# Optimization experiments

Measured on AMD Instinct MI355X. Metric: run time of the kernel, lower is better.

The kernel has to match this reference:

```python
import jax, jax.numpy as jnp
import numpy as np

B, I, C, H, QP, VP = 2, 1024, 16, 12, 4, 8
W_C = (2.0 / (9.0 * QP)) ** 0.5
W_L = (1.0 / 3.0) ** 0.5


def setup_inputs() -> dict:
    key = jax.random.key(0)
    ks = jax.random.split(key, 14)
    rn = lambda k, shape, s=1.0: (jax.random.normal(k, shape, dtype=jnp.float32) * s)
    return {
        "s": rn(ks[0], (B, I, C)),
        "z": rn(ks[1], (B, I, I, C)),
        "R": rn(ks[2], (B, I, 3, 3)),
        "t": rn(ks[3], (B, I, 3)),
        "Wq": rn(ks[4], (C, C * H), C ** -0.5),
        "Wk": rn(ks[5], (C, C * H), C ** -0.5),
        "Wv": rn(ks[6], (C, C * H), C ** -0.5),
        "Wb": rn(ks[7], (C, H), C ** -0.5),
        "Wqp": rn(ks[8], (C, 3 * QP * H), C ** -0.5),
        "Wkp": rn(ks[9], (C, 3 * QP * H), C ** -0.5),
        "Wvp": rn(ks[10], (C, 3 * VP * H), C ** -0.5),
        "gamma": rn(ks[11], (H,), 0.5),
        "Wout": rn(ks[12], (H * (2 * C + 4 * VP), C), (H * (2 * C + 4 * VP)) ** -0.5),
        "bout": rn(ks[13], (C,), 0.02),
    }


def _apply_rigid(R, t, p):
    # p: (B, i, n, 3); rigid transform per residue: R @ p + t
    return jnp.einsum("bixy,bipy->bipx", R, p) + t[:, :, None, :]


def reference(s, z, R, t, Wq, Wk, Wv, Wb, Wqp, Wkp, Wvp, gamma, Wout, bout):
    b_, i_, c = s.shape
    h, qp, vp = gamma.shape[0], Wqp.shape[1] // (3 * gamma.shape[0]), Wvp.shape[1] // (3 * gamma.shape[0])

    q = (s @ Wq).reshape(b_, i_, h, c)
    k = (s @ Wk).reshape(b_, i_, h, c)
    v = (s @ Wv).reshape(b_, i_, h, c)

    q_pts = _apply_rigid(R, t, (s @ Wqp).reshape(b_, i_, h * qp, 3)).reshape(b_, i_, h, qp, 3)
    k_pts = _apply_rigid(R, t, (s @ Wkp).reshape(b_, i_, h * qp, 3)).reshape(b_, i_, h, qp, 3)
    v_pts = _apply_rigid(R, t, (s @ Wvp).reshape(b_, i_, h * vp, 3)).reshape(b_, i_, h, vp, 3)

    bias = jnp.einsum("bijc,ch->bhij", z, Wb)
    a = jnp.einsum("bihc,bjhc->bhij", q, k) * (c ** -0.5) + bias

    # squared point distances summed over points, expanded to avoid (B,i,j,h,P,3) tensor
    q2 = jnp.sum(q_pts ** 2, axis=(-1, -2))          # (B,i,h)
    k2 = jnp.sum(k_pts ** 2, axis=(-1, -2))          # (B,j,h)
    qk = jnp.einsum("bihpx,bjhpx->bhij", q_pts, k_pts)
    d2 = q2.transpose(0, 2, 1)[..., None] + k2.transpose(0, 2, 1)[:, :, None, :] - 2.0 * qk  # (B,h,i,j)

    head_w = jax.nn.softplus(gamma)                  # (h,)
    a = a + d2 * (head_w[None, :, None, None] * W_C * -0.5)
    a = a * W_L
    a = jax.nn.softmax(a, axis=-2)  # NOTE: original code softmaxes over dim=-2 (the i axis)

    # NOTE: original einsum indexes v by i (not j); replicated faithfully
    o = jnp.einsum("bhij,bihc->bihc", a, v).reshape(b_, i_, h * c)

    o_pts = jnp.einsum("bhij,bjhpx->bihpx", a, v_pts)  # (B,i,h,vp,3)
    o_pts_norm = jnp.sqrt(jnp.maximum(jnp.sum(o_pts ** 2, axis=-1), 1e-12)).reshape(b_, i_, h * vp)
    o_pts_flat = o_pts.reshape(b_, i_, h * vp * 3)

    o_pair = jnp.einsum("bhij,bijc->bihc", a, z).reshape(b_, i_, h * c)

    cat = jnp.concatenate([o, o_pair, o_pts_flat, o_pts_norm], axis=-1)
    return cat @ Wout + bout
```

## Files before the change

kernel.cpp:

```cpp
#include <hip/hip_runtime.h>
#include <hip/hip_bf16.h>
#include <math.h>

#define B_ 2
#define I_ 1024
#define C_ 16
#define H_ 12
#define ICH 16

__device__ __constant__ float kW_C = 0.23570226039551584f;
#define W_Lc 0.5773502691896258f
#define LOG2E 1.4426950408889634f

typedef _Float16 hf;
typedef hf hf2 __attribute__((ext_vector_type(2)));
typedef hf hf4v __attribute__((ext_vector_type(4)));
typedef hf hf8v __attribute__((ext_vector_type(8)));
typedef float f32x4 __attribute__((ext_vector_type(4)));
typedef unsigned int u32;

template <typename T, typename F>
__device__ inline T bc(F f) { return __builtin_bit_cast(T, f); }

__device__ inline float fdot2f(u32 a, u32 b, float c) {
#if __has_builtin(__builtin_amdgcn_fdot2)
  return __builtin_amdgcn_fdot2(bc<hf2>(a), bc<hf2>(b), c, false);
#else
  hf2 x = bc<hf2>(a), y = bc<hf2>(b);
  return c + (float)x[0] * (float)y[0] + (float)x[1] * (float)y[1];
#endif
}

__device__ inline u32 pkrtz(float lo, float hi) {
#if __has_builtin(__builtin_amdgcn_cvt_pkrtz)
  return bc<u32>(__builtin_amdgcn_cvt_pkrtz(lo, hi));
#else
  hf2 t; t[0] = (hf)lo; t[1] = (hf)hi; return bc<u32>(t);
#endif
}

__device__ inline u32 permlo(u32 hiw, u32 low) {
#if __has_builtin(__builtin_amdgcn_perm)
  return __builtin_amdgcn_perm(hiw, low, 0x05040100u);
#else
  return (low & 0xffffu) | (hiw << 16);
#endif
}
__device__ inline u32 permhi(u32 hiw, u32 low) {
#if __has_builtin(__builtin_amdgcn_perm)
  return __builtin_amdgcn_perm(hiw, low, 0x07060302u);
#else
  return (low >> 16) | (hiw & 0xffff0000u);
#endif
}

#define QF16_OFF 0
#define QF16_SZ (B_*I_*196)
#define KF16_OFF (QF16_OFF + QF16_SZ)
#define KF16_SZ QF16_SZ
#define VPF_OFF (KF16_OFF + KF16_SZ)
#define VPF_SZ (B_*I_*144)
#define VV_OFF (VPF_OFF + VPF_SZ)
#define VV_SZ (B_*I_*192)
#define SM_OFF (VV_OFF + VV_SZ)
#define SM_SZ (B_*12*1024*2)
#define PM_OFF (SM_OFF + SM_SZ)
#define PM_SZ (B_*64*ICH*192*2)
#define LT_OFF (PM_OFF + PM_SZ)
#define LT_SZ (B_*H_*512*1024)
#define ACC2_OFF (LT_OFF + LT_SZ)

__global__ __launch_bounds__(192) void kA(const float* __restrict__ s, const float* __restrict__ R,
                 const float* __restrict__ t, const float* __restrict__ Wq,
                 const float* __restrict__ Wk, const float* __restrict__ Wv,
                 const float* __restrict__ Wqp, const float* __restrict__ Wkp,
                 const float* __restrict__ Wvp, const float* __restrict__ gam,
                 float* __restrict__ ws) {
  int blk = blockIdx.x;
  int b = blk >> 10, i = blk & 1023;
  int tid = threadIdx.x;
  __shared__ float sl[16], rl[9], tl[3], part[96];
  if (tid < 16) sl[tid] = s[(b*I_ + i)*C_ + tid];
  else if (tid < 25) rl[tid-16] = R[(size_t)(b*I_+i)*9 + (tid-16)];
  else if (tid < 28) tl[tid-25] = t[(size_t)(b*I_+i)*3 + (tid-25)];
  __syncthreads();
  hf* QF  = (hf*)(ws + QF16_OFF) + (size_t)(b*I_+i)*392;
  hf* KF  = (hf*)(ws + KF16_OFF) + (size_t)(b*I_+i)*392;
  ushort* VPP = (ushort*)(ws + VPF_OFF);
  float* vv = ws + VV_OFF + (size_t)(b*I_+i)*192;
  {
    int hc = tid; int h = hc >> 4, c = hc & 15;
    float aq = 0.f, ak = 0.f, av = 0.f;
    #pragma unroll
    for (int ci = 0; ci < 16; ci++) {
      float sv = sl[ci];
      aq += sv * Wq[ci*192 + hc];
      ak += sv * Wk[ci*192 + hc];
      av += sv * Wv[ci*192 + hc];
    }
    const float s_qk = 0.25f * W_Lc * LOG2E;
    QF[h*32 + c] = (hf)(aq * s_qk);
    KF[h*32 + c] = (hf)ak;
    vv[hc] = av;
  }
  {
    float raw[3], px[3];
    if (tid < 96) {
      bool isq = tid < 48;
      int n = isq ? tid : tid - 48;
      const float* W = isq ? Wqp : Wkp;
      #pragma unroll
      for (int x = 0; x < 3; x++) {
        float a2 = 0.f;
        #pragma unroll
        for (int ci = 0; ci < 16; ci++) a2 += sl[ci] * W[ci*144 + n*3 + x];
        raw[x] = a2;
      }
      #pragma unroll
      for (int x = 0; x < 3; x++)
        px[x] = rl[x*3]*raw[0] + rl[x*3+1]*raw[1] + rl[x*3+2]*raw[2] + tl[x];
      int h = n >> 2, p = n & 3;
      part[tid] = px[0]*px[0] + px[1]*px[1] + px[2]*px[2];
      if (isq) {
        float g = gam[h];
        float sp = log1pf(expf(g));
        float coef2 = -0.5f * kW_C * sp * W_Lc * LOG2E;
        #pragma unroll
        for (int x = 0; x < 3; x++) QF[h*32 + 16 + p*3 + x] = (hf)(px[x] * (-2.0f * coef2));
      } else {
        #pragma unroll
        for (int x = 0; x < 3; x++) KF[h*32 + 16 + p*3 + x] = (hf)px[x];
      }
    } else {
      int n = tid - 96;
      #pragma unroll
      for (int x = 0; x < 3; x++) {
        float a2 = 0.f;
        #pragma unroll
        for (int ci = 0; ci < 16; ci++) a2 += sl[ci] * Wvp[ci*288 + n*3 + x];
        raw[x] = a2;
      }
      #pragma unroll
      for (int x = 0; x < 3; x++)
        px[x] = rl[x*3]*raw[0] + rl[x*3+1]*raw[1] + rl[x*3+2]*raw[2] + tl[x];
      int h = n >> 3, p = n & 7;
      size_t base = ((size_t)(b*512 + (i >> 1))*12 + h)*48 + (i & 1);
      #pragma unroll
      for (int x = 0; x < 3; x++) VPP[base + (p*3 + x)*2] = bc<ushort>((hf)px[x]);
    }
  }
  __syncthreads();
  if (tid < 24) {
    int h = tid % 12; bool isq = tid < 12;
    float g = gam[h];
    float sp = log1pf(expf(g));
    float coef2 = -0.5f * kW_C * sp * W_Lc * LOG2E;
    float s2 = 0.f;
    int base = isq ? h*4 : 48 + h*4;
    #pragma unroll
    for (int p = 0; p < 4; p++) s2 += part[base + p];
    if (isq) {
      QF[h*32 + 28] = (hf)(coef2 * s2);
      QF[h*32 + 29] = (hf)1.0f;
      QF[h*32 + 30] = (hf)0.0f;
      QF[h*32 + 31] = (hf)0.0f;
    } else {
      KF[h*32 + 28] = (hf)1.0f;
      KF[h*32 + 29] = (hf)(coef2 * s2);
      KF[h*32 + 30] = (hf)0.0f;
      KF[h*32 + 31] = (hf)0.0f;
    }
  }
}

__global__ __launch_bounds__(256,6) void kB(const float* __restrict__ z,
                 const float* __restrict__ Wb, float* __restrict__ ws) {
  int blk = blockIdx.x;
  int ic = blk & (ICH-1); int jt = (blk >> 4) & 63; int b = blk >> 10;
  int tid = threadIdx.x;
  int w = tid >> 6, lane = tid & 63;
  int ln15 = lane & 15, l16 = lane >> 4;
  int j0 = jt*16;
  __shared__ u32 lqk[12*16*18];
  __shared__ u32 lbias32[16*112];
  const ushort* QFu = (const ushort*)(ws + QF16_OFF);
  const ushort* KFu = (const ushort*)(ws + KF16_OFF);
  hf8v kf[3];
  #pragma unroll
  for (int q = 0; q < 3; q++) {
    int h = w*3 + q;
    kf[q] = *(const hf8v*)&KFu[(size_t)(b*I_ + j0 + ln15)*392 + h*32 + l16*8];
  }
  hf4v wbf;
  #pragma unroll
  for (int e = 0; e < 4; e++) {
    int c = l16*4 + e;
    float v = (ln15 < 12) ? Wb[c*12 + ln15] * (W_Lc*LOG2E) : 0.f;
    wbf[e] = (hf)v;
  }
  u32* LTu_w = (u32*)(ws + LT_OFF);
  float m = -1e30f, S = 0.f;
  float4 zb0, zb1, zb2, zb3;
  {
    const float* zbase = z + ((size_t)(b*I_ + ic*64 + w*4)*I_ + j0 + ln15)*16 + l16*4;
    zb0 = *(const float4*)(zbase);
    zb1 = *(const float4*)(zbase + (size_t)I_*16);
    zb2 = *(const float4*)(zbase + (size_t)I_*32);
    zb3 = *(const float4*)(zbase + (size_t)I_*48);
  }
  for (int t = 0; t < 4; ++t) {
    int i0 = ic*64 + t*16;
    #pragma unroll
    for (int q = 0; q < 3; q++) {
      int h = w*3 + q;
      hf8v a = *(const hf8v*)&QFu[(size_t)(b*I_ + i0 + ln15)*392 + h*32 + l16*8];
      f32x4 c = {0.f, 0.f, 0.f, 0.f};
      c = __builtin_amdgcn_mfma_f32_16x16x32_f16(a, kf[q], c, 0, 0, 0);
      u32* dst = &lqk[(h*16 + ln15)*18 + l16*4];
      *(uint2*)dst     = make_uint2(bc<u32>(c[0]), bc<u32>(c[1]));
      *(uint2*)(dst+2) = make_uint2(bc<u32>(c[2]), bc<u32>(c[3]));
    }
    #pragma unroll
    for (int r = 0; r < 4; r++) {
      float4 zv = (r == 0) ? zb0 : (r == 1) ? zb1 : (r == 2) ? zb2 : zb3;
      int ii = w*4 + r;
      uint2 ap = make_uint2(pkrtz(zv.x, zv.y), pkrtz(zv.z, zv.w));
      hf4v a = bc<hf4v>(ap);
      f32x4 cb = {0.f, 0.f, 0.f, 0.f};
      cb = __builtin_amdgcn_mfma_f32_16x16x16f16(a, wbf, cb, 0, 0, 0);
      if (ln15 < 12) {
        u32 b01 = pkrtz(cb[0], cb[1]);
        u32 b23 = pkrtz(cb[2], cb[3]);
        *(uint2*)&lbias32[ii*112 + ln15*9 + l16*2] = make_uint2(b01, b23);
      }
    }
    if (t < 3) {
      const float* zbase = z + ((size_t)(b*I_ + ic*64 + (t+1)*16 + w*4)*I_ + j0 + ln15)*16 + l16*4;
      zb0 = *(const float4*)(zbase);
      zb1 = *(const float4*)(zbase + (size_t)I_*16);
      zb2 = *(const float4*)(zbase + (size_t)I_*32);
      zb3 = *(const float4*)(zbase + (size_t)I_*48);
    }
    __syncthreads();
    if (tid < 192) {
      int h = tid >> 4, jl = tid & 15;
      const u32* qk = &lqk[(h*16 + jl)*18];
      float l[16];
      #pragma unroll
      for (int i = 0; i < 16; i++) {
        u32 bb = lbias32[i*112 + h*9 + (jl >> 1)];
        ushort bu = (jl & 1) ? (ushort)(bb >> 16) : (ushort)(bb & 0xffffu);
        l[i] = bc<float>(qk[i]) + (float)bc<hf>(bu);
      }
      u32 lw[8];
      #pragma unroll
      for (int p = 0; p < 8; p++) lw[p] = pkrtz(l[2*p], l[2*p+1]);
      float lr[16];
      #pragma unroll
      for (int p = 0; p < 8; p++) { hf2 lh = bc<hf2>(lw[p]); lr[2*p] = (float)lh[0]; lr[2*p+1] = (float)lh[1]; }
      float m8[8];
      #pragma unroll
      for (int p = 0; p < 8; p++) m8[p] = fmaxf(lr[2*p], lr[2*p+1]);
      float mt = fmaxf(fmaxf(fmaxf(m8[0],m8[1]), fmaxf(m8[2],m8[3])),
                       fmaxf(fmaxf(m8[4],m8[5]), fmaxf(m8[6],m8[7])));
      float e[16];
      #pragma unroll
      for (int p = 0; p < 16; p++) e[p] = __builtin_amdgcn_exp2f(lr[p] - mt);
      float st = ((e[0]+e[1])+(e[2]+e[3])) + ((e[4]+e[5])+(e[6]+e[7]))
               + ((e[8]+e[9])+(e[10]+e[11])) + ((e[12]+e[13])+(e[14]+e[15]));
      float mn = fmaxf(m, mt);
      S = S * __builtin_amdgcn_exp2f(m - mn) + st * __builtin_amdgcn_exp2f(mt - mn);
      m = mn;
      u32 ex[8];
      #pragma unroll
      for (int p = 0; p < 8; p++) {
        u32 pw = (u32)__shfl_xor((int)lw[p], 1);
        ex[p] = (jl & 1) ? permhi(lw[p], pw) : permlo(pw, lw[p]);
      }
      u32 sw[8];
      #pragma unroll
      for (int p = 0; p < 8; p++) sw[p] = (u32)__shfl_xor((int)ex[p], 1);
      int par = jl & 1;
      u32 o0 = par ? sw[4] : ex[0];
      u32 o1 = par ? ex[4] : sw[0];
      u32 o2 = par ? sw[5] : ex[1];
      u32 o3 = par ? ex[5] : sw[1];
      u32 o4 = par ? sw[6] : ex[2];
      u32 o5 = par ? ex[6] : sw[2];
      u32 o6 = par ? sw[7] : ex[3];
      u32 o7 = par ? ex[7] : sw[3];
      u32* dst = LTu_w + ((size_t)(b*12+h)*512 + jt*8 + (jl>>1))*1024 + i0 + par*8;
      *(uint4*)dst     = make_uint4(o0, o1, o2, o3);
      *(uint4*)(dst+4) = make_uint4(o4, o5, o6, o7);
    }
    __syncthreads();
  }
  if (tid < 192) {
    float2* pm = (float2*)(ws + PM_OFF);
    pm[((size_t)(b*64+jt)*ICH + ic)*192 + tid] = make_float2(m, S);
  }
}

__global__ __launch_bounds__(192) void kB2(float* __restrict__ ws) {
  int blk = blockIdx.x; int jt = blk & 63, b = blk >> 6;
  int tid = threadIdx.x; int h = tid >> 4, jl = tid & 15;
  const float2* pm = (const float2*)(ws + PM_OFF) + (size_t)(b*64+jt)*ICH*192 + tid;
  float m = -1e30f, S = 0.f;
  #pragma unroll
  for (int ic = 0; ic < ICH; ic++) {
    float2 p = pm[ic*192];
    float mn = fmaxf(m, p.x);
    S = S * __builtin_amdgcn_exp2f(m - mn) + p.y * __builtin_amdgcn_exp2f(p.x - mn);
    m = mn;
  }
  int j = jt*16 + jl;
  float* sm = ws + SM_OFF + ((size_t)((b*12+h)*1024) + j)*2;
  sm[0] = m;
  sm[1] = 1.0f / S;
}

__global__ __launch_bounds__(192,6) void kC(const float* __restrict__ z,
                 float* __restrict__ ws, int jsh) {
  int blk = blockIdx.x;
  int jch = 1 << jsh;
  int jc = blk & (jch-1); int it = (blk >> jsh) & 63; int b = blk >> (jsh+6);
  int tid = threadIdx.x; int h = tid >> 4, il = tid & 15;
  int i = it*16 + il;
  __shared__ u32 llds[96*18];
  __shared__ u32 zplds[16*132];
  float opts[24], opair[16], rsum = 0.f;
  #pragma unroll
  for (int n = 0; n < 24; n++) opts[n] = 0.f;
  #pragma unroll
  for (int c = 0; c < 16; c++) opair[c] = 0.f;
  const u32* LTu = (const u32*)(ws + LT_OFF);
  const float* SM = ws + SM_OFF + (size_t)((b*12+h)*1024)*2;
  const ushort* VPP = (const ushort*)(ws + VPF_OFF);
  int chunk = I_ >> jsh;
  int nt = chunk >> 4;
  int hh = tid >> 4, rr = tid & 15, sjp = rr >> 1, sq = rr & 1;
  for (int t = 0; t < nt; ++t) {
    int j0 = jc*chunk + t*16;
    int jpg0 = j0 >> 1;
    __syncthreads();
    {
      const u32* src = LTu + ((size_t)(b*12+hh)*512 + jpg0 + sjp)*1024 + it*16 + sq*8;
      uint4 a = *(const uint4*)src;
      uint4 c4 = *(const uint4*)(src + 4);
      u32* drow = llds + (hh*8 + sjp)*18 + sq*8;
      *(uint2*)(drow + 0) = make_uint2(a.x, a.y);
      *(uint2*)(drow + 2) = make_uint2(a.z, a.w);
      *(uint2*)(drow + 4) = make_uint2(c4.x, c4.y);
      *(uint2*)(drow + 6) = make_uint2(c4.z, c4.w);
    }
    for (int idx = tid; idx < 512; idx += 192) {
      int r = idx >> 5, jp = (idx >> 2) & 7, c4 = idx & 3;
      const float* zb = z + ((size_t)(b*I_ + it*16 + r)*I_ + j0 + 2*jp)*16 + c4*4;
      float4 a = *(const float4*)zb;
      float4 d = *(const float4*)(zb + 16);
      uint4 o = make_uint4(pkrtz(a.x, d.x), pkrtz(a.y, d.y), pkrtz(a.z, d.z), pkrtz(a.w, d.w));
      *(uint4*)&zplds[r*132 + jp*16 + c4*4] = o;
    }
    __syncthreads();
    #pragma unroll 1
    for (int jp = 0; jp < 8; ++jp) {
      u32 lp = llds[(h*8 + jp)*18 + il];
      float4 st = *(const float4*)(SM + (size_t)(j0 + 2*jp)*2);
      const uint4* vp4 = (const uint4*)(VPP + ((size_t)(b*512 + jpg0 + jp)*12 + h)*48);
      uint4 va = vp4[0], vb = vp4[1], vc = vp4[2];
      uint4 vd = vp4[3], ve = vp4[4], vf = vp4[5];
      hf2 lh = bc<hf2>(lp);
      float w0 = __builtin_amdgcn_exp2f((float)lh[0] - st.x) * st.y;
      float w1 = __builtin_amdgcn_exp2f((float)lh[1] - st.z) * st.w;
      rsum += w0 + w1;
      u32 w2 = pkrtz(w0, w1);
      const u32* zr = &zplds[il*132 + jp*16];
      uint4 p0 = *(const uint4*)(zr + 0), p1 = *(const uint4*)(zr + 4);
      uint4 p2 = *(const uint4*)(zr + 8), p3 = *(const uint4*)(zr + 12);
      opair[0]  = fdot2f(w2, p0.x, opair[0]);
      opair[1]  = fdot2f(w2, p0.y, opair[1]);
      opair[2]  = fdot2f(w2, p0.z, opair[2]);
      opair[3]  = fdot2f(w2, p0.w, opair[3]);
      opair[4]  = fdot2f(w2, p1.x, opair[4]);
      opair[5]  = fdot2f(w2, p1.y, opair[5]);
      opair[6]  = fdot2f(w2, p1.z, opair[6]);
      opair[7]  = fdot2f(w2, p1.w, opair[7]);
      opair[8]  = fdot2f(w2, p2.x, opair[8]);
      opair[9]  = fdot2f(w2, p2.y, opair[9]);
      opair[10] = fdot2f(w2, p2.z, opair[10]);
      opair[11] = fdot2f(w2, p2.w, opair[11]);
      opair[12] = fdot2f(w2, p3.x, opair[12]);
      opair[13] = fdot2f(w2, p3.y, opair[13]);
      opair[14] = fdot2f(w2, p3.z, opair[14]);
      opair[15] = fdot2f(w2, p3.w, opair[15]);
      opts[0]  = fdot2f(w2, va.x, opts[0]);
      opts[1]  = fdot2f(w2, va.y, opts[1]);
      opts[2]  = fdot2f(w2, va.z, opts[2]);
      opts[3]  = fdot2f(w2, va.w, opts[3]);
      opts[4]  = fdot2f(w2, vb.x, opts[4]);
      opts[5]  = fdot2f(w2, vb.y, opts[5]);
      opts[6]  = fdot2f(w2, vb.z, opts[6]);
      opts[7]  = fdot2f(w2, vb.w, opts[7]);
      opts[8]  = fdot2f(w2, vc.x, opts[8]);
      opts[9]  = fdot2f(w2, vc.y, opts[9]);
      opts[10] = fdot2f(w2, vc.z, opts[10]);
      opts[11] = fdot2f(w2, vc.w, opts[11]);
      opts[12] = fdot2f(w2, vd.x, opts[12]);
      opts[13] = fdot2f(w2, vd.y, opts[13]);
      opts[14] = fdot2f(w2, vd.z, opts[14]);
      opts[15] = fdot2f(w2, vd.w, opts[15]);
      opts[16] = fdot2f(w2, ve.x, opts[16]);
      opts[17] = fdot2f(w2, ve.y, opts[17]);
      opts[18] = fdot2f(w2, ve.z, opts[18]);
      opts[19] = fdot2f(w2, ve.w, opts[19]);
      opts[20] = fdot2f(w2, vf.x, opts[20]);
      opts[21] = fdot2f(w2, vf.y, opts[21]);
      opts[22] = fdot2f(w2, vf.z, opts[22]);
      opts[23] = fdot2f(w2, vf.w, opts[23]);
    }
  }
  ushort* ab = (ushort*)(ws + ACC2_OFF) + ((size_t)(b*I_+i)*jch + jc)*512;
  #pragma unroll
  for (int n = 0; n < 24; n++) ab[h*24 + n] = bc<ushort>((hf)opts[n]);
  #pragma unroll
  for (int c = 0; c < 16; c++) ab[288 + h*16 + c] = bc<ushort>((hf)opair[c]);
  ab[480 + h] = bc<ushort>((hf)rsum);
}

__global__ __launch_bounds__(256) void kD(const float* __restrict__ Wout, const float* __restrict__ bout,
                 const float* __restrict__ ws, float* __restrict__ out, int jsh) {
  int jch = 1 << jsh;
  int blk = blockIdx.x;
  int b = blk >> 8; int i0 = (blk & 255) << 2;
  int tid = threadIdx.x;
  __shared__ float accs[4*512];
  __shared__ float cat[4*776];
  __shared__ float red[256];
  const ushort* ACC2us = (const ushort*)(ws + ACC2_OFF);
  for (int idx = tid; idx < 4*512; idx += 256) {
    int r = idx >> 9, f = idx & 511;
    const ushort* src = ACC2us + (size_t)(b*I_+i0+r)*jch*512 + f;
    float ssum = 0.f;
    for (int jc = 0; jc < jch; jc++) ssum += (float)bc<hf>(src[jc*512]);
    accs[idx] = ssum;
  }
  __syncthreads();
  const float* vv = ws + VV_OFF;
  for (int idx = tid; idx < 4*768; idx += 256) {
    int r = idx / 768, f = idx - r*768;
    int i = i0 + r;
    const float* ab = accs + r*512;
    float val;
    if (f < 192) {
      int h = f >> 4, c = f & 15;
      val = vv[(size_t)(b*I_+i)*192 + h*16 + c] * ab[480 + h];
    } else if (f < 384) {
      val = ab[288 + (f - 192)];
    } else if (f < 672) {
      val = ab[f - 384];
    } else {
      int g = f - 672; int base = (g >> 3)*24 + (g & 7)*3;
      float x0 = ab[base], x1 = ab[base+1], x2 = ab[base+2];
      val = sqrtf(fmaxf(x0*x0 + x1*x1 + x2*x2, 1e-12f));
    }
    cat[r*776 + f] = val;
  }
  __syncthreads();
  {
    int r = tid >> 6, c = (tid >> 2) & 15, sseg = tid & 3;
    const float* cr = cat + r*776;
    float a = 0.f;
    for (int f = sseg*192; f < sseg*192 + 192; f++) a += cr[f] * Wout[f*16 + c];
    red[tid] = a;
  }
  __syncthreads();
  if ((tid & 3) == 0) {
    int r = tid >> 6, c = (tid >> 2) & 15;
    float sum = bout[c] + red[tid] + red[tid+1] + red[tid+2] + red[tid+3];
    out[((size_t)(b*I_) + i0 + r)*16 + c] = sum;
  }
}

extern "C" void kernel_launch(void* const* d_in, const int* in_sizes, int n_in,
                              void* d_out, int out_size, void* d_ws, size_t ws_size,
                              hipStream_t stream) {
  const float* s    = (const float*)d_in[0];
  const float* z    = (const float*)d_in[1];
  const float* R    = (const float*)d_in[2];
  const float* t    = (const float*)d_in[3];
  const float* Wq   = (const float*)d_in[4];
  const float* Wk   = (const float*)d_in[5];
  const float* Wv   = (const float*)d_in[6];
  const float* Wb   = (const float*)d_in[7];
  const float* Wqp  = (const float*)d_in[8];
  const float* Wkp  = (const float*)d_in[9];
  const float* Wvp  = (const float*)d_in[10];
  const float* gam  = (const float*)d_in[11];
  const float* Wout = (const float*)d_in[12];
  const float* bout = (const float*)d_in[13];
  float* out = (float*)d_out;
  float* ws = (float*)d_ws;

  int jsh = 4;
  while (jsh > 0) {
    size_t need = ((size_t)ACC2_OFF + (size_t)B_*I_*(1u<<jsh)*256) * 4u;
    if (need <= ws_size) break;
    jsh--;
  }

  hipLaunchKernelGGL(kA, dim3(B_*I_), dim3(192), 0, stream,
                     s, R, t, Wq, Wk, Wv, Wqp, Wkp, Wvp, gam, ws);
  hipLaunchKernelGGL(kB, dim3(B_*64*ICH), dim3(256), 0, stream, z, Wb, ws);
  hipLaunchKernelGGL(kB2, dim3(B_*64), dim3(192), 0, stream, ws);
  hipLaunchKernelGGL(kC, dim3(B_*64*(1<<jsh)), dim3(192), 0, stream, z, ws, jsh);
  hipLaunchKernelGGL(kD, dim3(B_*256), dim3(256), 0, stream, Wout, bout, ws, out, jsh);
}
```

Measured before the change: 180.0 us.

## Double-buffer LDS tiles in kC with register prefetch of next z/logit tile

kC now keeps two LDS buffers for the logit and z tiles. The next tile's global loads are issued into registers before the current tile's compute loop and written to the other buffer afterward. This overlaps global memory latency with the dot-product work and removes one barrier per iteration. It lowers the launch-bounds occupancy hint from 6 to 3 to make room for the extra prefetch registers, and it unrolls the inner loop by 2, at the cost of fewer resident waves and double the LDS use.

```diff
diff --git a/kernel.cpp b/kernel.cpp
--- a/kernel.cpp
+++ b/kernel.cpp
@@ -319,15 +319,15 @@
   sm[1] = 1.0f / S;
 }
 
-__global__ __launch_bounds__(192,6) void kC(const float* __restrict__ z,
+__global__ __launch_bounds__(192,3) void kC(const float* __restrict__ z,
                  float* __restrict__ ws, int jsh) {
   int blk = blockIdx.x;
   int jch = 1 << jsh;
   int jc = blk & (jch-1); int it = (blk >> jsh) & 63; int b = blk >> (jsh+6);
   int tid = threadIdx.x; int h = tid >> 4, il = tid & 15;
   int i = it*16 + il;
-  __shared__ u32 llds[96*18];
-  __shared__ u32 zplds[16*132];
+  __shared__ u32 llds[2][96*18];
+  __shared__ u32 zplds[2][16*132];
   float opts[24], opair[16], rsum = 0.f;
   #pragma unroll
   for (int n = 0; n < 24; n++) opts[n] = 0.f;
@@ -339,32 +339,60 @@
   int chunk = I_ >> jsh;
   int nt = chunk >> 4;
   int hh = tid >> 4, rr = tid & 15, sjp = rr >> 1, sq = rr & 1;
+  int x0r = tid >> 5,        x0jp = (tid >> 2) & 7,        x0c = tid & 3;
+  int x1r = (tid+192) >> 5,  x1jp = ((tid+192) >> 2) & 7,  x1c = (tid+192) & 3;
+  int x2r = (tid+384) >> 5,  x2jp = ((tid+384) >> 2) & 7,  x2c = (tid+384) & 3;
+  uint4 lta, ltb;
+  float4 za0, zd0, za1, zd1, za2, zd2;
+  {
+    int j0 = jc*chunk;
+    int jpg0 = j0 >> 1;
+    const u32* src = LTu + ((size_t)(b*12+hh)*512 + jpg0 + sjp)*1024 + it*16 + sq*8;
+    lta = *(const uint4*)src;
+    ltb = *(const uint4*)(src + 4);
+    const float* zb0p = z + ((size_t)(b*I_ + it*16 + x0r)*I_ + j0 + 2*x0jp)*16 + x0c*4;
+    za0 = *(const float4*)zb0p; zd0 = *(const float4*)(zb0p + 16);
+    const float* zb1p = z + ((size_t)(b*I_ + it*16 + x1r)*I_ + j0 + 2*x1jp)*16 + x1c*4;
+    za1 = *(const float4*)zb1p; zd1 = *(const float4*)(zb1p + 16);
+    if (tid < 128) {
+      const float* zb2p = z + ((size_t)(b*I_ + it*16 + x2r)*I_ + j0 + 2*x2jp)*16 + x2c*4;
+      za2 = *(const float4*)zb2p; zd2 = *(const float4*)(zb2p + 16);
+    }
+    u32* drow = llds[0] + (hh*8 + sjp)*18 + sq*8;
+    *(uint2*)(drow + 0) = make_uint2(lta.x, lta.y);
+    *(uint2*)(drow + 2) = make_uint2(lta.z, lta.w);
+    *(uint2*)(drow + 4) = make_uint2(ltb.x, ltb.y);
+    *(uint2*)(drow + 6) = make_uint2(ltb.z, ltb.w);
+    *(uint4*)&zplds[0][x0r*132 + x0jp*16 + x0c*4] =
+      make_uint4(pkrtz(za0.x, zd0.x), pkrtz(za0.y, zd0.y), pkrtz(za0.z, zd0.z), pkrtz(za0.w, zd0.w));
+    *(uint4*)&zplds[0][x1r*132 + x1jp*16 + x1c*4] =
+      make_uint4(pkrtz(za1.x, zd1.x), pkrtz(za1.y, zd1.y), pkrtz(za1.z, zd1.z), pkrtz(za1.w, zd1.w));
+    if (tid < 128)
+      *(uint4*)&zplds[0][x2r*132 + x2jp*16 + x2c*4] =
+        make_uint4(pkrtz(za2.x, zd2.x), pkrtz(za2.y, zd2.y), pkrtz(za2.z, zd2.z), pkrtz(za2.w, zd2.w));
+    __syncthreads();
+  }
   for (int t = 0; t < nt; ++t) {
+    int cur = t & 1;
     int j0 = jc*chunk + t*16;
     int jpg0 = j0 >> 1;
-    __syncthreads();
-    {
-      const u32* src = LTu + ((size_t)(b*12+hh)*512 + jpg0 + sjp)*1024 + it*16 + sq*8;
-      uint4 a = *(const uint4*)src;
-      uint4 c4 = *(const uint4*)(src + 4);
-      u32* drow = llds + (hh*8 + sjp)*18 + sq*8;
-      *(uint2*)(drow + 0) = make_uint2(a.x, a.y);
-      *(uint2*)(drow + 2) = make_uint2(a.z, a.w);
-      *(uint2*)(drow + 4) = make_uint2(c4.x, c4.y);
-      *(uint2*)(drow + 6) = make_uint2(c4.z, c4.w);
-    }
-    for (int idx = tid; idx < 512; idx += 192) {
-      int r = idx >> 5, jp = (idx >> 2) & 7, c4 = idx & 3;
-      const float* zb = z + ((size_t)(b*I_ + it*16 + r)*I_ + j0 + 2*jp)*16 + c4*4;
-      float4 a = *(const float4*)zb;
-      float4 d = *(const float4*)(zb + 16);
-      uint4 o = make_uint4(pkrtz(a.x, d.x), pkrtz(a.y, d.y), pkrtz(a.z, d.z), pkrtz(a.w, d.w));
-      *(uint4*)&zplds[r*132 + jp*16 + c4*4] = o;
-    }
-    __syncthreads();
-    #pragma unroll 1
+    if (t + 1 < nt) {
+      int j1 = j0 + 16;
+      const u32* src = LTu + ((size_t)(b*12+hh)*512 + (j1>>1) + sjp)*1024 + it*16 + sq*8;
+      lta = *(const uint4*)src;
+      ltb = *(const uint4*)(src + 4);
+      const float* zb0p = z + ((size_t)(b*I_ + it*16 + x0r)*I_ + j1 + 2*x0jp)*16 + x0c*4;
+      za0 = *(const float4*)zb0p; zd0 = *(const float4*)(zb0p + 16);
+      const float* zb1p = z + ((size_t)(b*I_ + it*16 + x1r)*I_ + j1 + 2*x1jp)*16 + x1c*4;
+      za1 = *(const float4*)zb1p; zd1 = *(const float4*)(zb1p + 16);
+      if (tid < 128) {
+        const float* zb2p = z + ((size_t)(b*I_ + it*16 + x2r)*I_ + j1 + 2*x2jp)*16 + x2c*4;
+        za2 = *(const float4*)zb2p; zd2 = *(const float4*)(zb2p + 16);
+      }
+    }
+    #pragma unroll 2
     for (int jp = 0; jp < 8; ++jp) {
-      u32 lp = llds[(h*8 + jp)*18 + il];
+      u32 lp = llds[cur][(h*8 + jp)*18 + il];
       float4 st = *(const float4*)(SM + (size_t)(j0 + 2*jp)*2);
       const uint4* vp4 = (const uint4*)(VPP + ((size_t)(b*512 + jpg0 + jp)*12 + h)*48);
       uint4 va = vp4[0], vb = vp4[1], vc = vp4[2];
@@ -374,7 +402,7 @@
       float w1 = __builtin_amdgcn_exp2f((float)lh[1] - st.z) * st.w;
       rsum += w0 + w1;
       u32 w2 = pkrtz(w0, w1);
-      const u32* zr = &zplds[il*132 + jp*16];
+      const u32* zr = &zplds[cur][il*132 + jp*16];
       uint4 p0 = *(const uint4*)(zr + 0), p1 = *(const uint4*)(zr + 4);
       uint4 p2 = *(const uint4*)(zr + 8), p3 = *(const uint4*)(zr + 12);
       opair[0]  = fdot2f(w2, p0.x, opair[0]);
@@ -418,6 +446,22 @@
       opts[22] = fdot2f(w2, vf.z, opts[22]);
       opts[23] = fdot2f(w2, vf.w, opts[23]);
     }
+    if (t + 1 < nt) {
+      int nb = cur ^ 1;
+      u32* drow = llds[nb] + (hh*8 + sjp)*18 + sq*8;
+      *(uint2*)(drow + 0) = make_uint2(lta.x, lta.y);
+      *(uint2*)(drow + 2) = make_uint2(lta.z, lta.w);
+      *(uint2*)(drow + 4) = make_uint2(ltb.x, ltb.y);
+      *(uint2*)(drow + 6) = make_uint2(ltb.z, ltb.w);
+      *(uint4*)&zplds[nb][x0r*132 + x0jp*16 + x0c*4] =
+        make_uint4(pkrtz(za0.x, zd0.x), pkrtz(za0.y, zd0.y), pkrtz(za0.z, zd0.z), pkrtz(za0.w, zd0.w));
+      *(uint4*)&zplds[nb][x1r*132 + x1jp*16 + x1c*4] =
+        make_uint4(pkrtz(za1.x, zd1.x), pkrtz(za1.y, zd1.y), pkrtz(za1.z, zd1.z), pkrtz(za1.w, zd1.w));
+      if (tid < 128)
+        *(uint4*)&zplds[nb][x2r*132 + x2jp*16 + x2c*4] =
+          make_uint4(pkrtz(za2.x, zd2.x), pkrtz(za2.y, zd2.y), pkrtz(za2.z, zd2.z), pkrtz(za2.w, zd2.w));
+      __syncthreads();
+    }
   }
   ushort* ab = (ushort*)(ws + ACC2_OFF) + ((size_t)(b*I_+i)*jch + jc)*512;
   #pragma unroll
```

New measurement: 171.6 us. 1.05x faster.
